# Optimization experiments

Measured on AMD Instinct MI355X. Metric: run time of the kernel, lower is better.

## Reference

```python
import jax, jax.numpy as jnp
import numpy as np

N_NODES = 100000
N_EDGES = 1600000
D_IN, D_HID, D_OUT = 128, 128, 64


def _mean_agg(h_src_feat, src, dst, num_nodes):
    # gather source features along edges, scatter-sum into destinations,
    # divide by in-degree (clamped to 1, matching DGL zero-degree handling)
    summed = jax.ops.segment_sum(h_src_feat[src], dst, num_segments=num_nodes)
    deg = jax.ops.segment_sum(jnp.ones((src.shape[0],), h_src_feat.dtype), dst,
                              num_segments=num_nodes)
    return summed / jnp.maximum(deg, 1.0)[:, None]


def setup_inputs() -> dict:
    key = jax.random.key(0)
    ks = jax.random.split(key, 8)
    x = jax.random.normal(ks[0], (N_NODES, D_IN), dtype=jnp.float32)
    src = jax.random.randint(ks[1], (N_EDGES,), 0, N_NODES, dtype=jnp.int64)
    dst = jax.random.randint(ks[2], (N_EDGES,), 0, N_NODES, dtype=jnp.int64)
    s1 = 1.0 / np.sqrt(D_IN)
    s2 = 1.0 / np.sqrt(D_HID)
    W_self1 = jax.random.normal(ks[3], (D_IN, D_HID), dtype=jnp.float32) * s1
    W_neigh1 = jax.random.normal(ks[4], (D_IN, D_HID), dtype=jnp.float32) * s1
    b1 = jnp.zeros((D_HID,), dtype=jnp.float32)
    W_self2 = jax.random.normal(ks[5], (D_HID, D_OUT), dtype=jnp.float32) * s2
    W_neigh2 = jax.random.normal(ks[6], (D_HID, D_OUT), dtype=jnp.float32) * s2
    b2 = jnp.zeros((D_OUT,), dtype=jnp.float32)
    return {"x": x, "src": src, "dst": dst,
            "W_self1": W_self1, "W_neigh1": W_neigh1, "b1": b1,
            "W_self2": W_self2, "W_neigh2": W_neigh2, "b2": b2}


def reference(x, src, dst, W_self1, W_neigh1, b1, W_self2, W_neigh2, b2):
    n = x.shape[0]
    # layer 1: SAGEConv(mean) + ReLU (dropout is identity in eval mode)
    agg1 = _mean_agg(x, src, dst, n)
    h = x @ W_self1 + agg1 @ W_neigh1 + b1
    h = jax.nn.relu(h)
    # layer 2: SAGEConv(mean)
    agg2 = _mean_agg(h, src, dst, n)
    out = h @ W_self2 + agg2 @ W_neigh2 + b2
    return out
```

## Files before the change

### kernel.cpp

```cpp
#include <hip/hip_runtime.h>

#define N_NODES 100000
#define N_EDGES 1600000
#define D 128
#define D_OUT 64
#define MAXDEG 64

#define NBUCK 782
#define BSHIFT 7
#define BCAP  3072
#define NBLK_SPLIT 500
#define CHUNK 3200
#define NBLK_PACK 25

typedef __attribute__((ext_vector_type(8))) short short8;
typedef __attribute__((ext_vector_type(4))) float floatx4;
typedef __attribute__((ext_vector_type(2))) float floatx2;

__device__ inline unsigned short f2bf(float f) {
    unsigned u = __builtin_bit_cast(unsigned, f);
    u = (u + 0x7fffu + ((u >> 16) & 1u)) >> 16;
    return (unsigned short)u;
}
__device__ inline float bf2f(unsigned u16) {
    return __builtin_bit_cast(float, u16 << 16);
}

template<bool KPERM>
__device__ inline void pack_ncat(const float* __restrict__ Wa, const float* __restrict__ Wb,
                                 int ncA, int ncB, unsigned short* __restrict__ out, int t) {
    int nnt = (ncA + ncB) >> 4;
    int lane = t & 63;
    int nt = (t >> 6) % nnt;
    int kt = t / (64 * nnt);
    int col = nt * 16 + (lane & 15);
    int k0 = kt * 32 + ((lane >> 4) << 3);
    const float* W = (col < ncA) ? Wa : Wb;
    int nc = (col < ncA) ? ncA : ncB;
    int c  = (col < ncA) ? col : col - ncA;
    unsigned short* dstp = out + (size_t)((kt * nnt + nt) * 64 + lane) * 8;
    #pragma unroll
    for (int j = 0; j < 8; ++j) {
        int k = k0 + j;
        int kr = KPERM ? (((k & 7) << 4) | (k >> 3)) : k;
        dstp[j] = f2bf(W[(size_t)kr * nc + c]);
    }
}

__global__ __launch_bounds__(256) void split_pack(
        const int* __restrict__ src, const int* __restrict__ dst,
        int* __restrict__ gcur, int* __restrict__ bucketbuf,
        const float* __restrict__ Ws1, const float* __restrict__ Wn1,
        const float* __restrict__ Ws2, const float* __restrict__ Wn2,
        unsigned short* __restrict__ Wp1, unsigned short* __restrict__ Wp2,
        unsigned char* __restrict__ y8, unsigned char* __restrict__ z8) {
    __shared__ int cnt[NBUCK];
    __shared__ int base_s[NBUCK];
    __shared__ int dstc[CHUNK];
    const int tid = threadIdx.x;
    const int b = blockIdx.x;
    if (b < NBLK_SPLIT) {
        const int e0 = b * CHUNK;
        for (int i = tid; i < NBUCK; i += 256) cnt[i] = 0;
        __syncthreads();
        for (int i = tid; i < CHUNK; i += 256) {
            int d = __builtin_nontemporal_load(dst + e0 + i);
            dstc[i] = d;
            atomicAdd(&cnt[d >> BSHIFT], 1);
        }
        __syncthreads();
        for (int i = tid; i < NBUCK; i += 256) {
            int c = cnt[i];
            base_s[i] = c ? atomicAdd(&gcur[i], c) : 0;
            cnt[i] = 0;
        }
        __syncthreads();
        for (int i = tid; i < CHUNK; i += 256) {
            int d = dstc[i];
            int s = __builtin_nontemporal_load(src + e0 + i);
            int bk = d >> BSHIFT;
            int p = base_s[bk] + atomicAdd(&cnt[bk], 1);
            if (p < BCAP)
                bucketbuf[bk * BCAP + p] = ((d & 127) << 17) | s;
        }
    } else {
        int sub = b - NBLK_SPLIT;
        if (sub < 16)      pack_ncat<false>(Ws1, Wn1, D, D, Wp1, sub * 256 + tid);
        else if (sub < 24) pack_ncat<true >(Ws2, Wn2, D_OUT, D_OUT, Wp2, (sub - 16) * 256 + tid);
        else {
            if (tid < 32)       ((unsigned*)(y8 + (size_t)N_NODES * 128))[tid] = 0;
            else if (tid < 48)  ((unsigned*)(z8 + (size_t)N_NODES * 64))[tid - 32] = 0;
        }
    }
}

__global__ __launch_bounds__(256) void csr_build(
        const int* __restrict__ gcur, const int* __restrict__ bucketbuf,
        int* __restrict__ dcount, int* __restrict__ csrp) {
    __shared__ int lcnt[128];
    const int tid = threadIdx.x, b = blockIdx.x;
    if (tid < 128) lcnt[tid] = 0;
    __syncthreads();
    int m = gcur[b]; if (m > BCAP) m = BCAP;
    const int* __restrict__ buf = bucketbuf + b * BCAP;
    for (int i = tid; i < m; i += 256) {
        int v = buf[i];
        int dloc = (v >> 17) & 127, s = v & 0x1FFFF;
        int node = (b << BSHIFT) + dloc;
        int slot = atomicAdd(&lcnt[dloc], 1);
        if (slot < MAXDEG && node < N_NODES)
            csrp[((size_t)node << 6) + slot] = s;
    }
    __syncthreads();
    if (tid < 128) {
        int node = (b << BSHIFT) + tid;
        if (node < N_NODES) {
            int c = lcnt[tid]; if (c > MAXDEG) c = MAXDEG;
            dcount[node] = c;
            int cf = (c + 15) & ~15; if (cf > MAXDEG) cf = MAXDEG;
            int* row = csrp + ((size_t)node << 6);
            for (int k = c; k < cf; ++k) row[k] = N_NODES;
        }
    }
}

template<int NTA, int NTB, bool AF32, bool OUTA_BF16, bool ILV>
__global__ __launch_bounds__(256) void gemm_dual(
        const void* __restrict__ A, const unsigned short* __restrict__ Wp,
        const float* __restrict__ bias, void* __restrict__ OutA,
        unsigned char* __restrict__ OutB)
{
    const int NT = NTA + NTB;
    const int wave = threadIdx.x >> 6;
    const int lane = threadIdx.x & 63;
    const int q = lane >> 4, m = lane & 15;

    int row = blockIdx.x * 64 + wave * 16 + m;
    int rowc = (row < N_NODES) ? row : (N_NODES - 1);

    floatx4 acc[NT];
    #pragma unroll
    for (int nt = 0; nt < NT; ++nt) acc[nt] = (floatx4){0.f, 0.f, 0.f, 0.f};

    #pragma unroll
    for (int kt = 0; kt < 4; ++kt) {
        short8 af;
        if (AF32) {
            const float* xr = (const float*)A + (size_t)rowc * D + kt * 32 + q * 8;
            float4 f0 = *(const float4*)xr;
            float4 f1 = *(const float4*)(xr + 4);
            af[0] = (short)f2bf(f0.x); af[1] = (short)f2bf(f0.y);
            af[2] = (short)f2bf(f0.z); af[3] = (short)f2bf(f0.w);
            af[4] = (short)f2bf(f1.x); af[5] = (short)f2bf(f1.y);
            af[6] = (short)f2bf(f1.z); af[7] = (short)f2bf(f1.w);
        } else {
            af = *(const short8*)((const unsigned short*)A +
                                  (size_t)rowc * D + kt * 32 + q * 8);
        }
        #pragma unroll
        for (int nt = 0; nt < NT; ++nt) {
            short8 bf = *(const short8*)(Wp + (size_t)((kt * NT + nt) * 64 + lane) * 8);
            acc[nt] = __builtin_amdgcn_mfma_f32_16x16x32_bf16(af, bf, acc[nt], 0, 0, 0);
        }
    }

    const int orow_base = blockIdx.x * 64 + wave * 16 + q * 4;
    if (ILV) {
        float bv[8];
        #pragma unroll
        for (int nt = 0; nt < 8; ++nt) bv[nt] = bias[nt * 16 + m];
        #pragma unroll
        for (int i = 0; i < 4; ++i) {
            int orow = orow_base + i;
            if (orow < N_NODES) {
                unsigned w[4];
                #pragma unroll
                for (int t = 0; t < 4; ++t) {
                    float v0 = acc[2 * t][i]     + bv[2 * t];
                    float v1 = acc[2 * t + 1][i] + bv[2 * t + 1];
                    w[t] = (unsigned)f2bf(v0) | ((unsigned)f2bf(v1) << 16);
                }
                uint4 pv; pv.x = w[0]; pv.y = w[1]; pv.z = w[2]; pv.w = w[3];
                *(uint4*)((unsigned short*)OutA + (size_t)orow * 128 + m * 8) = pv;
                int pk0 = __builtin_amdgcn_cvt_pk_fp8_f32(acc[8][i],  acc[9][i],  0,   false);
                pk0     = __builtin_amdgcn_cvt_pk_fp8_f32(acc[10][i], acc[11][i], pk0, true);
                int pk1 = __builtin_amdgcn_cvt_pk_fp8_f32(acc[12][i], acc[13][i], 0,   false);
                pk1     = __builtin_amdgcn_cvt_pk_fp8_f32(acc[14][i], acc[15][i], pk1, true);
                uint2 v8; v8.x = (unsigned)pk0; v8.y = (unsigned)pk1;
                *(uint2*)(OutB + (size_t)orow * 128 + m * 8) = v8;
            }
        }
    } else {
        #pragma unroll
        for (int nt = 0; nt < NT; ++nt) {
            float bv = (nt < NTA) ? bias[nt * 16 + m] : 0.f;
            #pragma unroll
            for (int i = 0; i < 4; ++i) {
                int orow = orow_base + i;
                if (orow < N_NODES) {
                    float v = acc[nt][i];
                    if (nt < NTA) {
                        v += bv;
                        if (OUTA_BF16)
                            ((unsigned short*)OutA)[(size_t)orow * (NTA * 16) + nt * 16 + m] = f2bf(v);
                        else
                            ((float*)OutA)[(size_t)orow * (NTA * 16) + nt * 16 + m] = v;
                    } else {
                        int pk = __builtin_amdgcn_cvt_pk_fp8_f32(v, v, 0, false);
                        OutB[(size_t)orow * (NTB * 16) + (nt - NTA) * 16 + m] =
                            (unsigned char)(pk & 0xff);
                    }
                }
            }
        }
    }
}

template<bool L1>
__global__ __launch_bounds__(256) void agg_add(
        const unsigned char* __restrict__ feat, const int* __restrict__ csrp,
        const int* __restrict__ dcount, const void* __restrict__ self,
        void* __restrict__ out)
{
    const int LPE = L1 ? 32 : 16;
    const int EPG = 64 / LPE;
    const int FSH = L1 ? 7 : 6;
    const int NC  = L1 ? 128 : 64;

    int w = (blockIdx.x * 256 + threadIdx.x) >> 6;
    int lane = threadIdx.x & 63;
    if (w >= N_NODES) return;
    int dg = __builtin_amdgcn_readfirstlane(dcount[w]);
    const int g = lane / LPE;
    const int l = lane % LPE;
    int idxv = csrp[((size_t)w << 6) + lane];

    floatx2 ac0 = (floatx2){0.f, 0.f};
    floatx2 ac1 = (floatx2){0.f, 0.f};
    for (int j = 0; j < dg; j += 16) {
        #pragma unroll
        for (int u = 0; u < 16 / EPG; ++u) {
            int s = __shfl(idxv, j + u * EPG + g);
            unsigned v = *(const unsigned*)(feat + ((size_t)s << FSH) + (l << 2));
            ac0 += __builtin_amdgcn_cvt_pk_f32_fp8(v, false);
            ac1 += __builtin_amdgcn_cvt_pk_f32_fp8(v, true);
        }
    }
    #pragma unroll
    for (int delta = 32; delta >= LPE; delta >>= 1) {
        ac0.x += __shfl_down(ac0.x, delta); ac0.y += __shfl_down(ac0.y, delta);
        ac1.x += __shfl_down(ac1.x, delta); ac1.y += __shfl_down(ac1.y, delta);
    }
    if (g == 0) {
        float invd = (dg > 0) ? 1.0f / (float)dg : 1.0f;
        if (L1) {
            uint2 sv = *(const uint2*)((const unsigned short*)self + (size_t)w * NC + l * 4);
            float h0 = bf2f(sv.x & 0xffffu)  + ac0.x * invd;
            float h1 = bf2f(sv.x >> 16)      + ac0.y * invd;
            float h2 = bf2f(sv.y & 0xffffu)  + ac1.x * invd;
            float h3 = bf2f(sv.y >> 16)      + ac1.y * invd;
            h0 = fmaxf(h0, 0.f); h1 = fmaxf(h1, 0.f);
            h2 = fmaxf(h2, 0.f); h3 = fmaxf(h3, 0.f);
            uint2 pv;
            pv.x = (unsigned)f2bf(h0) | ((unsigned)f2bf(h1) << 16);
            pv.y = (unsigned)f2bf(h2) | ((unsigned)f2bf(h3) << 16);
            *(uint2*)((unsigned short*)out + (size_t)w * NC + l * 4) = pv;
        } else {
            const float* sp = (const float*)self + (size_t)w * NC + l * 4;
            float4 s0 = *(const float4*)sp;
            float4 o;
            o.x = s0.x + ac0.x * invd; o.y = s0.y + ac0.y * invd;
            o.z = s0.z + ac1.x * invd; o.w = s0.w + ac1.y * invd;
            *(float4*)((float*)out + (size_t)w * NC + l * 4) = o;
        }
    }
}

extern "C" void kernel_launch(void* const* d_in, const int* in_sizes, int n_in,
                              void* d_out, int out_size, void* d_ws, size_t ws_size,
                              hipStream_t stream) {
    const float* x   = (const float*)d_in[0];
    const int*   src = (const int*)d_in[1];
    const int*   dst = (const int*)d_in[2];
    const float* Ws1 = (const float*)d_in[3];
    const float* Wn1 = (const float*)d_in[4];
    const float* b1  = (const float*)d_in[5];
    const float* Ws2 = (const float*)d_in[6];
    const float* Wn2 = (const float*)d_in[7];
    const float* b2  = (const float*)d_in[8];
    float* out = (float*)d_out;

    const size_t nd = (size_t)N_NODES * D;
    unsigned short* h   = (unsigned short*)d_ws;
    unsigned short* xs  = h + nd;
    float*          tmp = (float*)xs;
    unsigned char*  y8  = (unsigned char*)(xs + nd);
    unsigned char*  z8  = y8 + (size_t)(N_NODES + 1) * D;
    int* dcount = (int*)(z8 + (size_t)(N_NODES + 1) * D_OUT);
    int* csrp   = dcount + N_NODES;
    int* gcur   = csrp + (size_t)N_NODES * MAXDEG;
    int* bucketbuf = gcur + 1024;
    unsigned short* Wp1 = (unsigned short*)(bucketbuf + (size_t)NBUCK * BCAP);
    unsigned short* Wp2 = Wp1 + 32768;

    hipMemsetAsync(gcur, 0, NBUCK * sizeof(int), stream);

    split_pack<<<NBLK_SPLIT + NBLK_PACK, 256, 0, stream>>>(
        src, dst, gcur, bucketbuf, Ws1, Wn1, Ws2, Wn2, Wp1, Wp2, y8, z8);
    csr_build<<<NBUCK, 256, 0, stream>>>(gcur, bucketbuf, dcount, csrp);

    const int gemm_blocks = (N_NODES + 63) / 64;
    const int agg_blocks  = (N_NODES * 64 + 255) / 256;

    gemm_dual<8, 8, true,  true,  true ><<<gemm_blocks, 256, 0, stream>>>(x, Wp1, b1, xs, y8);
    agg_add<true ><<<agg_blocks, 256, 0, stream>>>(y8, csrp, dcount, xs, h);
    gemm_dual<4, 4, false, false, false><<<gemm_blocks, 256, 0, stream>>>(h, Wp2, b2, tmp, z8);
    agg_add<false><<<agg_blocks, 256, 0, stream>>>(z8, csrp, dcount, tmp, out);
}
```

Measured before the change: 286.7 us.

## Fuse CSR build into layer-1 GEMM launch and vectorize layer-2 GEMM epilogue

The CSR bucket-to-row build now runs as extra blocks of the layer-1 GEMM kernel. This removes one launch and lets the index building overlap with the dense GEMM work. The layer-2 GEMM epilogue now writes float4 and packed 4-byte fp8 stores in a column-interleaved layout instead of scalar byte and float stores. The layer-2 aggregation reads that interleaved layout and writes the final output with strided scalar stores. The aggregation kernels also skip loading CSR index slots beyond the padded degree, trading some output-store coalescing for fewer and wider GEMM stores.

```diff
diff --git a/kernel.cpp b/kernel.cpp
--- a/kernel.cpp
+++ b/kernel.cpp
@@ -12,6 +12,7 @@
 #define NBLK_SPLIT 500
 #define CHUNK 3200
 #define NBLK_PACK 25
+#define GEMM_BLOCKS 1563
 
 typedef __attribute__((ext_vector_type(8))) short short8;
 typedef __attribute__((ext_vector_type(4))) float floatx4;
@@ -94,48 +95,18 @@
     }
 }
 
-__global__ __launch_bounds__(256) void csr_build(
-        const int* __restrict__ gcur, const int* __restrict__ bucketbuf,
-        int* __restrict__ dcount, int* __restrict__ csrp) {
-    __shared__ int lcnt[128];
-    const int tid = threadIdx.x, b = blockIdx.x;
-    if (tid < 128) lcnt[tid] = 0;
-    __syncthreads();
-    int m = gcur[b]; if (m > BCAP) m = BCAP;
-    const int* __restrict__ buf = bucketbuf + b * BCAP;
-    for (int i = tid; i < m; i += 256) {
-        int v = buf[i];
-        int dloc = (v >> 17) & 127, s = v & 0x1FFFF;
-        int node = (b << BSHIFT) + dloc;
-        int slot = atomicAdd(&lcnt[dloc], 1);
-        if (slot < MAXDEG && node < N_NODES)
-            csrp[((size_t)node << 6) + slot] = s;
-    }
-    __syncthreads();
-    if (tid < 128) {
-        int node = (b << BSHIFT) + tid;
-        if (node < N_NODES) {
-            int c = lcnt[tid]; if (c > MAXDEG) c = MAXDEG;
-            dcount[node] = c;
-            int cf = (c + 15) & ~15; if (cf > MAXDEG) cf = MAXDEG;
-            int* row = csrp + ((size_t)node << 6);
-            for (int k = c; k < cf; ++k) row[k] = N_NODES;
-        }
-    }
-}
-
-template<int NTA, int NTB, bool AF32, bool OUTA_BF16, bool ILV>
-__global__ __launch_bounds__(256) void gemm_dual(
+template<int NTA, int NTB, bool AF32, int ILV>
+__device__ inline void gemm_body(int bid,
         const void* __restrict__ A, const unsigned short* __restrict__ Wp,
         const float* __restrict__ bias, void* __restrict__ OutA,
-        unsigned char* __restrict__ OutB)
+        unsigned char* __restrict__ OutB, int tid)
 {
     const int NT = NTA + NTB;
-    const int wave = threadIdx.x >> 6;
-    const int lane = threadIdx.x & 63;
+    const int wave = tid >> 6;
+    const int lane = tid & 63;
     const int q = lane >> 4, m = lane & 15;
 
-    int row = blockIdx.x * 64 + wave * 16 + m;
+    int row = bid * 64 + wave * 16 + m;
     int rowc = (row < N_NODES) ? row : (N_NODES - 1);
 
     floatx4 acc[NT];
@@ -164,8 +135,8 @@
         }
     }
 
-    const int orow_base = blockIdx.x * 64 + wave * 16 + q * 4;
-    if (ILV) {
+    const int orow_base = bid * 64 + wave * 16 + q * 4;
+    if (ILV == 1) {
         float bv[8];
         #pragma unroll
         for (int nt = 0; nt < 8; ++nt) bv[nt] = bias[nt * 16 + m];
@@ -191,29 +162,70 @@
             }
         }
     } else {
-        #pragma unroll
-        for (int nt = 0; nt < NT; ++nt) {
-            float bv = (nt < NTA) ? bias[nt * 16 + m] : 0.f;
-            #pragma unroll
-            for (int i = 0; i < 4; ++i) {
-                int orow = orow_base + i;
-                if (orow < N_NODES) {
-                    float v = acc[nt][i];
-                    if (nt < NTA) {
-                        v += bv;
-                        if (OUTA_BF16)
-                            ((unsigned short*)OutA)[(size_t)orow * (NTA * 16) + nt * 16 + m] = f2bf(v);
-                        else
-                            ((float*)OutA)[(size_t)orow * (NTA * 16) + nt * 16 + m] = v;
-                    } else {
-                        int pk = __builtin_amdgcn_cvt_pk_fp8_f32(v, v, 0, false);
-                        OutB[(size_t)orow * (NTB * 16) + (nt - NTA) * 16 + m] =
-                            (unsigned char)(pk & 0xff);
-                    }
-                }
+        float bv[4];
+        #pragma unroll
+        for (int nt = 0; nt < 4; ++nt) bv[nt] = bias[nt * 16 + m];
+        #pragma unroll
+        for (int i = 0; i < 4; ++i) {
+            int orow = orow_base + i;
+            if (orow < N_NODES) {
+                float4 o;
+                o.x = acc[0][i] + bv[0]; o.y = acc[1][i] + bv[1];
+                o.z = acc[2][i] + bv[2]; o.w = acc[3][i] + bv[3];
+                *(float4*)((float*)OutA + (size_t)orow * 64 + m * 4) = o;
+                int pk = __builtin_amdgcn_cvt_pk_fp8_f32(acc[4][i], acc[5][i], 0,  false);
+                pk     = __builtin_amdgcn_cvt_pk_fp8_f32(acc[6][i], acc[7][i], pk, true);
+                *(unsigned*)(OutB + (size_t)orow * 64 + m * 4) = (unsigned)pk;
             }
         }
     }
+}
+
+__global__ __launch_bounds__(256) void gemm1_csr(
+        const float* __restrict__ x, const unsigned short* __restrict__ Wp1,
+        const float* __restrict__ b1, unsigned short* __restrict__ xs,
+        unsigned char* __restrict__ y8,
+        const int* __restrict__ gcur, const int* __restrict__ bucketbuf,
+        int* __restrict__ dcount, int* __restrict__ csrp)
+{
+    __shared__ int lcnt[128];
+    const int tid = threadIdx.x;
+    if (blockIdx.x < GEMM_BLOCKS) {
+        gemm_body<8, 8, true, 1>(blockIdx.x, x, Wp1, b1, xs, y8, tid);
+    } else {
+        const int b = blockIdx.x - GEMM_BLOCKS;
+        if (tid < 128) lcnt[tid] = 0;
+        __syncthreads();
+        int m = gcur[b]; if (m > BCAP) m = BCAP;
+        const int* __restrict__ buf = bucketbuf + b * BCAP;
+        for (int i = tid; i < m; i += 256) {
+            int v = buf[i];
+            int dloc = (v >> 17) & 127, s = v & 0x1FFFF;
+            int node = (b << BSHIFT) + dloc;
+            int slot = atomicAdd(&lcnt[dloc], 1);
+            if (slot < MAXDEG && node < N_NODES)
+                csrp[((size_t)node << 6) + slot] = s;
+        }
+        __syncthreads();
+        if (tid < 128) {
+            int node = (b << BSHIFT) + tid;
+            if (node < N_NODES) {
+                int c = lcnt[tid]; if (c > MAXDEG) c = MAXDEG;
+                dcount[node] = c;
+                int cf = (c + 15) & ~15; if (cf > MAXDEG) cf = MAXDEG;
+                int* row = csrp + ((size_t)node << 6);
+                for (int k = c; k < cf; ++k) row[k] = N_NODES;
+            }
+        }
+    }
+}
+
+__global__ __launch_bounds__(256) void gemm2(
+        const unsigned short* __restrict__ h, const unsigned short* __restrict__ Wp2,
+        const float* __restrict__ b2, float* __restrict__ tmp,
+        unsigned char* __restrict__ z8)
+{
+    gemm_body<4, 4, false, 2>(blockIdx.x, h, Wp2, b2, tmp, z8, threadIdx.x);
 }
 
 template<bool L1>
@@ -231,9 +243,11 @@
     int lane = threadIdx.x & 63;
     if (w >= N_NODES) return;
     int dg = __builtin_amdgcn_readfirstlane(dcount[w]);
+    int cf = (dg + 15) & ~15;
     const int g = lane / LPE;
     const int l = lane % LPE;
-    int idxv = csrp[((size_t)w << 6) + lane];
+    int idxv = 0;
+    if (lane < cf) idxv = csrp[((size_t)w << 6) + lane];
 
     floatx2 ac0 = (floatx2){0.f, 0.f};
     floatx2 ac1 = (floatx2){0.f, 0.f};
@@ -268,10 +282,15 @@
         } else {
             const float* sp = (const float*)self + (size_t)w * NC + l * 4;
             float4 s0 = *(const float4*)sp;
-            float4 o;
-            o.x = s0.x + ac0.x * invd; o.y = s0.y + ac0.y * invd;
-            o.z = s0.z + ac1.x * invd; o.w = s0.w + ac1.y * invd;
-            *(float4*)((float*)out + (size_t)w * NC + l * 4) = o;
+            float v0 = s0.x + ac0.x * invd;
+            float v1 = s0.y + ac0.y * invd;
+            float v2 = s0.z + ac1.x * invd;
+            float v3 = s0.w + ac1.y * invd;
+            float* op = (float*)out + (size_t)w * NC;
+            op[l]      = v0;
+            op[16 + l] = v1;
+            op[32 + l] = v2;
+            op[48 + l] = v3;
         }
     }
 }
@@ -307,13 +326,12 @@
 
     split_pack<<<NBLK_SPLIT + NBLK_PACK, 256, 0, stream>>>(
         src, dst, gcur, bucketbuf, Ws1, Wn1, Ws2, Wn2, Wp1, Wp2, y8, z8);
-    csr_build<<<NBUCK, 256, 0, stream>>>(gcur, bucketbuf, dcount, csrp);
-
-    const int gemm_blocks = (N_NODES + 63) / 64;
-    const int agg_blocks  = (N_NODES * 64 + 255) / 256;
-
-    gemm_dual<8, 8, true,  true,  true ><<<gemm_blocks, 256, 0, stream>>>(x, Wp1, b1, xs, y8);
+
+    const int agg_blocks = (N_NODES * 64 + 255) / 256;
+
+    gemm1_csr<<<GEMM_BLOCKS + NBUCK, 256, 0, stream>>>(
+        x, Wp1, b1, xs, y8, gcur, bucketbuf, dcount, csrp);
     agg_add<true ><<<agg_blocks, 256, 0, stream>>>(y8, csrp, dcount, xs, h);
-    gemm_dual<4, 4, false, false, false><<<gemm_blocks, 256, 0, stream>>>(h, Wp2, b2, tmp, z8);
+    gemm2<<<GEMM_BLOCKS, 256, 0, stream>>>(h, Wp2, b2, tmp, z8);
     agg_add<false><<<agg_blocks, 256, 0, stream>>>(z8, csrp, dcount, tmp, out);
 }
```

After: 274.7 us. -4.2%, faster.
